# Kernel optimization log

Measured on AMD Instinct MI355X. Metric: run time of the kernel, lower is better.

Reference implementation:

```python
import jax, jax.numpy as jnp
import numpy as np

N = 100000      # num nodes
E = 3200000     # num edges (avg degree 32)
F = 512         # num_features
D = 256         # args.dim
C = 64          # num_classes
K = 10          # APPNP iterations
ALPHA = 0.1


def setup_inputs() -> dict:
    key = jax.random.key(0)
    ks = jax.random.split(key, 6)
    x = jax.random.normal(ks[0], (N, F), dtype=jnp.float32)
    edge_index = jax.random.randint(ks[1], (2, E), 0, N, dtype=jnp.int64)
    edge_weight_train = jax.random.normal(ks[2], (E,), dtype=jnp.float32)
    x_weight = jnp.ones((F,), dtype=jnp.float32)
    W1 = jax.random.normal(ks[3], (F, D), dtype=jnp.float32) * 0.02
    b1 = jnp.zeros((D,), dtype=jnp.float32)
    W2 = jax.random.normal(ks[4], (D, C), dtype=jnp.float32) * 0.02
    b2 = jnp.zeros((C,), dtype=jnp.float32)
    return {"x": x, "edge_index": edge_index, "edge_weight_train": edge_weight_train,
            "x_weight": x_weight, "W1": W1, "b1": b1, "W2": W2, "b2": b2}


def reference(x, edge_index, edge_weight_train, x_weight, W1, b1, W2, b2):
    row, col = edge_index[0], edge_index[1]
    # adj_sparse branch: mask edges with |w|==0, weight = sigmoid(w).
    # Filtering edges == zeroing their weight (degrees and messages scale by w).
    edge_mask = jnp.abs(edge_weight_train) > 0
    w = jnp.where(edge_mask, jax.nn.sigmoid(edge_weight_train), 0.0)
    # gcn_norm with self-loops (fill value 1.0)
    loop = jnp.arange(N, dtype=row.dtype)
    row2 = jnp.concatenate([row, loop])
    col2 = jnp.concatenate([col, loop])
    w2 = jnp.concatenate([w, jnp.ones((N,), dtype=w.dtype)])
    deg = jax.ops.segment_sum(w2, col2, num_segments=N)
    dinv = jnp.where(deg > 0, jax.lax.rsqrt(jnp.maximum(deg, 1e-12)), 0.0)
    norm = dinv[row2] * w2 * dinv[col2]  # [E+N]

    # feature_sparse branch
    x_mask = (jnp.abs(x_weight) > 0).astype(x.dtype)
    xw = jax.nn.sigmoid(x_weight) * x_mask
    xin = x * xw  # broadcast over nodes

    h = jax.nn.relu(xin @ W1 + b1)          # [N, D] (dropout is eval no-op)
    z0 = h @ W2 + b2                        # [N, C]

    z = z0
    for _ in range(K):
        msg = z[row2] * norm[:, None]       # gather + scale, [E+N, C]
        agg = jax.ops.segment_sum(msg, col2, num_segments=N)
        z = (1.0 - ALPHA) * agg + ALPHA * z0
    return jax.nn.log_softmax(z, axis=1)
```

## Files before the change

kernel.cpp:

```cpp
#include <hip/hip_runtime.h>
#include <hip/hip_bf16.h>
#include <cstdint>
#include <cstddef>

#define ALPHA 0.1f
#define K_ITERS 10
#define NPART 8

typedef __attribute__((ext_vector_type(8))) short bf16x8;
typedef __attribute__((ext_vector_type(4))) float f32x4;
typedef __attribute__((ext_vector_type(4))) unsigned int u32x4;

#define U15INV (1.0f / 32767.0f)

__device__ __forceinline__ unsigned short f2bf(float f) {
    unsigned int u = __float_as_uint(f);
    u += 0x7fffu + ((u >> 16) & 1u);
    return (unsigned short)(u >> 16);
}
__device__ __forceinline__ float bflo(unsigned int u) {
    return __uint_as_float(u << 16);
}
__device__ __forceinline__ float bfhi(unsigned int u) {
    return __uint_as_float(u & 0xffff0000u);
}
__device__ __forceinline__ unsigned int pack2(float a, float b) {
    return (unsigned int)f2bf(a) | ((unsigned int)f2bf(b) << 16);
}
__device__ __forceinline__ unsigned int u15q(float w) {
    return (unsigned int)(w * 32767.0f + 0.5f);
}
__device__ __forceinline__ int xcd_id() {
    unsigned int x;
    asm volatile("s_getreg_b32 %0, hwreg(20, 0, 32)" : "=s"(x));
    return (int)(x & (NPART - 1));
}


__global__ __launch_bounds__(256) void setup_k(int* cntp, unsigned int* cs, int* flag,
                                               int ncnt, int ncs) {
    int i = blockIdx.x * 256 + threadIdx.x;
    if (i == 0) *flag = 0;
    if (i < ncnt) cntp[i] = 0;
    if (i < ncs) cs[i] = 0;
}

__global__ void detect_idx_k(const void* ei, int* flag, int E_, int N_) {
    int tid = threadIdx.x;
    const long long* p = (const long long*)ei;
    int bad = 0;
    int lim = (E_ < 4096) ? E_ : 4096;
    for (int i = tid; i < lim; i += 256) {
        long long v = p[i];
        if (v < 0 || v >= (long long)N_) bad = 1;
    }
    if (bad) atomicOr(flag, 1);
}

__global__ __launch_bounds__(256) void wprep_k(const float* W1, const float* xw, unsigned short* W1bT,
                                               const float* W2, unsigned short* W2bT,
                                               int F_, int D_, int C_) {
    int i = blockIdx.x * 256 + threadIdx.x;
    int n1 = F_ * D_;
    if (i < n1) {
        int k = i / D_, n = i % D_;
        float t = xw[k];
        float s = (fabsf(t) > 0.0f) ? 1.0f / (1.0f + expf(-t)) : 0.0f;
        W1bT[(size_t)n * F_ + k] = f2bf(W1[i] * s);
    } else if (i < n1 + D_ * C_) {
        int j = i - n1;
        int k = j / C_, n = j % C_;
        W2bT[(size_t)n * D_ + k] = f2bf(W2[j]);
    }
}

__global__ __launch_bounds__(512) void mlp_prep_k(
        const float* __restrict__ A, const unsigned short* __restrict__ BT,
        const float* __restrict__ b1, const unsigned short* __restrict__ W2bT,
        const float* __restrict__ b2, unsigned short* __restrict__ z0out,
        int M, int K, int Nn, int Cn, int gx,
        const void* __restrict__ ei, const float* __restrict__ ew,
        unsigned long long* __restrict__ epack, int* __restrict__ cntp,
        const int* __restrict__ flag, int E_, int N_) {
    __shared__ __align__(16) unsigned short SMEM[32768];

    if (blockIdx.x >= gx) {
        int e = (blockIdx.x - gx) * 512 + threadIdx.x;
        if (e >= E_) return;
        int is32 = *flag;
        unsigned long long r, c;
        if (is32) {
            const int* p = (const int*)ei;
            r = (unsigned long long)(unsigned int)p[e];
            c = (unsigned long long)(unsigned int)p[(size_t)E_ + e];
        } else {
            const long long* p = (const long long*)ei;
            r = (unsigned long long)p[e];
            c = (unsigned long long)p[(size_t)E_ + e];
        }
        float t = ew[e];
        float wv = (fabsf(t) > 0.0f) ? 1.0f / (1.0f + expf(-t)) : 0.0f;
        unsigned long long part = (unsigned long long)xcd_id();
        unsigned long long rk = (unsigned long long)(unsigned int)
            __hip_atomic_fetch_add(&cntp[(size_t)part * N_ + (int)c], 1,
                                   __ATOMIC_RELAXED, __HIP_MEMORY_SCOPE_WORKGROUP);
        epack[e] = r | (c << 17) | ((unsigned long long)u15q(wv) << 34)
                     | (part << 49) | (rk << 52);
        return;
    }

    const int BK = 32;
    typedef unsigned short (*AslT)[4][128][8];
    typedef unsigned short (*BslT)[4][256][8];
    AslT Asl = (AslT)SMEM;
    BslT Bsl = (BslT)(SMEM + 8192);

    int tid = threadIdx.x;
    int row0 = blockIdx.x * 128;
    int wid = tid >> 6, lane = tid & 63;
    int wm = wid & 1, wn = wid >> 1;
    int lrow = lane & 15, kg = lane >> 4;

    f32x4 acc[4][4];
    #pragma unroll
    for (int i = 0; i < 4; ++i)
        #pragma unroll
        for (int j = 0; j < 4; ++j) acc[i][j] = (f32x4){0.f, 0.f, 0.f, 0.f};

    int ar = tid >> 2, akg = tid & 3;
    int agrow = row0 + ar;
    bool avalid = agrow < M;
    int bn_ = tid >> 1, bkh = (tid & 1) * 16;

    float fa[8];
    bf16x8 bv0, bv1;

    auto loadTile = [&](int k0) {
        if (avalid) {
            const f32x4* p = (const f32x4*)&A[(size_t)agrow * K + k0 + akg * 8];
            *(f32x4*)&fa[0] = p[0];
            *(f32x4*)&fa[4] = p[1];
        }
        const bf16x8* p = (const bf16x8*)&BT[(size_t)bn_ * K + k0 + bkh];
        bv0 = p[0]; bv1 = p[1];
    };
    auto stageTile = [&](int buf) {
        unsigned short av[8];
        #pragma unroll
        for (int q = 0; q < 8; ++q) av[q] = avalid ? f2bf(fa[q]) : (unsigned short)0;
        *(bf16x8*)&Asl[buf][akg][ar][0] = *(bf16x8*)&av[0];
        *(bf16x8*)&Bsl[buf][(bkh >> 3) + 0][bn_][0] = bv0;
        *(bf16x8*)&Bsl[buf][(bkh >> 3) + 1][bn_][0] = bv1;
    };

    int nsteps = K / BK;
    loadTile(0);
    stageTile(0);
    __syncthreads();

    int cur = 0;
    for (int step = 0; step < nsteps; ++step) {
        bool more = (step + 1) < nsteps;
        if (more) loadTile((step + 1) * BK);

        bf16x8 af[4], bfr[4];
        #pragma unroll
        for (int i = 0; i < 4; ++i)
            af[i] = *(bf16x8*)&Asl[cur][kg][wm * 64 + i * 16 + lrow][0];
        #pragma unroll
        for (int j = 0; j < 4; ++j)
            bfr[j] = *(bf16x8*)&Bsl[cur][kg][wn * 64 + j * 16 + lrow][0];
        #pragma unroll
        for (int i = 0; i < 4; ++i)
            #pragma unroll
            for (int j = 0; j < 4; ++j)
                acc[i][j] = __builtin_amdgcn_mfma_f32_16x16x32_bf16(af[i], bfr[j], acc[i][j], 0, 0, 0);

        if (more) stageTile(cur ^ 1);
        __syncthreads();
        cur ^= 1;
    }

    #pragma unroll
    for (int i = 0; i < 4; ++i) {
        #pragma unroll
        for (int j = 0; j < 4; ++j) {
            int k2 = wn * 64 + j * 16 + lrow;
            float bv = b1[k2];
            int base = ((k2 >> 5) * 4 + ((k2 >> 3) & 3)) * 1024 + (k2 & 7);
            #pragma unroll
            for (int r = 0; r < 4; ++r) {
                int row = wm * 64 + i * 16 + kg * 4 + r;
                float v = fmaxf(acc[i][j][r] + bv, 0.0f);
                SMEM[base + row * 8] = f2bf(v);
            }
        }
    }
    __syncthreads();

    f32x4 acc2[4];
    #pragma unroll
    for (int i = 0; i < 4; ++i) acc2[i] = (f32x4){0.f, 0.f, 0.f, 0.f};
    int col2 = wn * 16 + lrow;
    #pragma unroll
    for (int ch = 0; ch < 8; ++ch) {
        bf16x8 bfr2 = *(const bf16x8*)&W2bT[(size_t)col2 * Nn + ch * 32 + kg * 8];
        bf16x8 af2[4];
        #pragma unroll
        for (int i = 0; i < 4; ++i)
            af2[i] = *(bf16x8*)&SMEM[(ch * 4 + kg) * 1024 + (wm * 64 + i * 16 + lrow) * 8];
        #pragma unroll
        for (int i = 0; i < 4; ++i)
            acc2[i] = __builtin_amdgcn_mfma_f32_16x16x32_bf16(af2[i], bfr2, acc2[i], 0, 0, 0);
    }
    float bv2 = b2[col2];
    #pragma unroll
    for (int i = 0; i < 4; ++i) {
        #pragma unroll
        for (int r = 0; r < 4; ++r) {
            int grow = row0 + wm * 64 + i * 16 + kg * 4 + r;
            if (grow < M)
                z0out[(size_t)grow * Cn + col2] = f2bf(acc2[i][r] + bv2);
        }
    }
}

__global__ __launch_bounds__(256) void combine_k(const int* cntp, int* pofs, int* cnt8, int N_) {
    int i = blockIdx.x * 256 + threadIdx.x;
    if (i >= N_) return;
    int s = 0;
    #pragma unroll
    for (int p = 0; p < NPART; ++p) {
        size_t idx = (size_t)p * N_ + i;
        int v = cntp[idx];
        pofs[idx] = s;
        s += v;
    }
    cnt8[i] = (s + 7) & ~7;
}

__global__ __launch_bounds__(256) void scan1_k(const int* cnt, int* bsum, int N_) {
    __shared__ int sm[256];
    int t = threadIdx.x, i = blockIdx.x * 256 + t;
    sm[t] = (i < N_) ? cnt[i] : 0;
    __syncthreads();
    for (int off = 128; off; off >>= 1) {
        if (t < off) sm[t] += sm[t + off];
        __syncthreads();
    }
    if (t == 0) bsum[blockIdx.x] = sm[0];
}

__global__ __launch_bounds__(1024) void scan2_k(const int* bsum, int* boff, int nb) {
    __shared__ int sm[1024];
    int t = threadIdx.x;
    int v = (t < nb) ? bsum[t] : 0;
    sm[t] = v;
    __syncthreads();
    for (int off = 1; off < 1024; off <<= 1) {
        int x = (t >= off) ? sm[t - off] : 0;
        __syncthreads();
        sm[t] += x;
        __syncthreads();
    }
    if (t < nb) boff[t] = sm[t] - v;
}

__global__ __launch_bounds__(256) void scan3_k(const int* cnt, const int* boff, int* rowstart, int N_) {
    __shared__ int sm[256];
    int t = threadIdx.x, i = blockIdx.x * 256 + t;
    int v = (i < N_) ? cnt[i] : 0;
    sm[t] = v;
    __syncthreads();
    for (int off = 1; off < 256; off <<= 1) {
        int x = (t >= off) ? sm[t - off] : 0;
        __syncthreads();
        sm[t] += x;
        __syncthreads();
    }
    if (i < N_)  rowstart[i]  = boff[blockIdx.x] + sm[t] - v;
    if (i == N_ - 1) rowstart[N_] = boff[blockIdx.x] + sm[t];
}

__global__ __launch_bounds__(256) void fill_csr_k(const unsigned long long* epack, const int* pofs,
                                                  const int* rowstart, unsigned int* cs,
                                                  int E_, int N_) {
    int e = blockIdx.x * 256 + threadIdx.x;
    if (e >= E_) return;
    unsigned long long v = epack[e];
    unsigned int r   = (unsigned int)(v & 0x1ffffu);
    int          c   = (int)((v >> 17) & 0x1ffffu);
    unsigned int w15 = (unsigned int)((v >> 34) & 0x7fffu);
    int         part = (int)((v >> 49) & 7u);
    int           rk = (int)(v >> 52);
    int pos = rowstart[c] + pofs[(size_t)part * N_ + c] + rk;
    cs[pos] = r | (w15 << 17);
}

__global__ __launch_bounds__(256) void deg_dinv_k(const unsigned int* __restrict__ cs,
                                                  const int* __restrict__ rowstart,
                                                  float* __restrict__ dinv, int N_) {
    int node = blockIdx.x * 8 + (threadIdx.x >> 5);
    int l = threadIdx.x & 31;
    if (node >= N_) return;
    int s = rowstart[node], e = rowstart[node + 1];
    float sum = 0.0f;
    for (int j = s + l; j < e; j += 32) sum += (float)(cs[j] >> 17) * U15INV;
    #pragma unroll
    for (int off = 16; off; off >>= 1) sum += __shfl_xor(sum, off, 64);
    float d = sum + 1.0f;
    if (l == 0) dinv[node] = (d > 0.0f) ? rsqrtf(fmaxf(d, 1e-12f)) : 0.0f;
}

__global__ __launch_bounds__(256) void norm_k(unsigned int* __restrict__ cs,
                                              const int* __restrict__ rowstart,
                                              const float* __restrict__ dinv, int N_) {
    int node = blockIdx.x * 8 + (threadIdx.x >> 5);
    int l = threadIdx.x & 31;
    if (node >= N_) return;
    int s = rowstart[node], e = rowstart[node + 1];
    float dc = dinv[node];
    for (int j = s + l; j < e; j += 32) {
        unsigned int v = cs[j];
        unsigned int src = v & 0x1ffffu;
        float w = (float)(v >> 17) * U15INV;
        float nm = dinv[src] * w * dc;
        cs[j] = src | (u15q(nm) << 17);
    }
}

template<bool LAST>
__global__ __launch_bounds__(256) void prop8_k(const unsigned short* __restrict__ z,
                                               const unsigned short* __restrict__ z0,
                                               const int* __restrict__ rowstart,
                                               const unsigned int* __restrict__ cs,
                                               const float* __restrict__ dinv,
                                               unsigned short* __restrict__ znew,
                                               float* __restrict__ out, int N_) {
    int node = blockIdx.x * 32 + (threadIdx.x >> 3);
    int l = threadIdx.x & 7;
    if (node >= N_) return;
    int s = rowstart[node], e = rowstart[node + 1];
    float d = dinv[node];
    size_t ro = (size_t)node * 64 + l * 8;
    u32x4 zs = *(const u32x4*)&z[ro];
    float dd = d * d;
    float a[8];
    a[0] = dd * bflo(zs.x); a[1] = dd * bfhi(zs.x);
    a[2] = dd * bflo(zs.y); a[3] = dd * bfhi(zs.y);
    a[4] = dd * bflo(zs.z); a[5] = dd * bfhi(zs.z);
    a[6] = dd * bflo(zs.w); a[7] = dd * bfhi(zs.w);

    for (int j = s; j < e; j += 8) {
        u32x4 p0 = __builtin_nontemporal_load((const u32x4*)&cs[j]);
        u32x4 p1 = __builtin_nontemporal_load((const u32x4*)&cs[j + 4]);
        unsigned int pe[8] = { p0.x, p0.y, p0.z, p0.w, p1.x, p1.y, p1.z, p1.w };
        u32x4 g[8];
        #pragma unroll
        for (int q = 0; q < 8; ++q)
            g[q] = *(const u32x4*)&z[(size_t)(pe[q] & 0x1ffffu) * 64 + l * 8];
        #pragma unroll
        for (int q = 0; q < 8; ++q) {
            float w = (float)(pe[q] >> 17) * U15INV;
            a[0] += w * bflo(g[q].x); a[1] += w * bfhi(g[q].x);
            a[2] += w * bflo(g[q].y); a[3] += w * bfhi(g[q].y);
            a[4] += w * bflo(g[q].z); a[5] += w * bfhi(g[q].z);
            a[6] += w * bflo(g[q].w); a[7] += w * bfhi(g[q].w);
        }
    }

    u32x4 z0v = __builtin_nontemporal_load((const u32x4*)&z0[ro]);
    float v[8];
    float z0f[8] = { bflo(z0v.x), bfhi(z0v.x), bflo(z0v.y), bfhi(z0v.y),
                     bflo(z0v.z), bfhi(z0v.z), bflo(z0v.w), bfhi(z0v.w) };
    #pragma unroll
    for (int q = 0; q < 8; ++q) v[q] = (1.0f - ALPHA) * a[q] + ALPHA * z0f[q];

    if (!LAST) {
        u32x4 o;
        o.x = pack2(v[0], v[1]); o.y = pack2(v[2], v[3]);
        o.z = pack2(v[4], v[5]); o.w = pack2(v[6], v[7]);
        *(u32x4*)&znew[ro] = o;
    } else {
        float m = v[0];
        #pragma unroll
        for (int q = 1; q < 8; ++q) m = fmaxf(m, v[q]);
        #pragma unroll
        for (int off = 1; off < 8; off <<= 1) m = fmaxf(m, __shfl_xor(m, off, 64));
        float sum = 0.0f;
        #pragma unroll
        for (int q = 0; q < 8; ++q) sum += expf(v[q] - m);
        #pragma unroll
        for (int off = 1; off < 8; off <<= 1) sum += __shfl_xor(sum, off, 64);
        float lg = logf(sum);
        float4 o0 = make_float4(v[0] - m - lg, v[1] - m - lg, v[2] - m - lg, v[3] - m - lg);
        float4 o1 = make_float4(v[4] - m - lg, v[5] - m - lg, v[6] - m - lg, v[7] - m - lg);
        *(float4*)&out[ro] = o0;
        *(float4*)&out[ro + 4] = o1;
    }
}


extern "C" void kernel_launch(void* const* d_in, const int* in_sizes, int n_in,
                              void* d_out, int out_size, void* d_ws, size_t ws_size,
                              hipStream_t stream) {
    const float* x   = (const float*)d_in[0];
    const void*  ei  = d_in[1];
    const float* ew  = (const float*)d_in[2];
    const float* xw  = (const float*)d_in[3];
    const float* W1  = (const float*)d_in[4];
    const float* b1  = (const float*)d_in[5];
    const float* W2  = (const float*)d_in[6];
    const float* b2  = (const float*)d_in[7];

    const int F_ = in_sizes[3];
    const int N_ = in_sizes[0] / F_;
    const int E_ = in_sizes[2];
    const int D_ = in_sizes[5];
    const int C_ = in_sizes[7];

    const int E8 = E_ + 7 * N_;

    char* base = (char*)d_ws;
    size_t off = 0;
    auto take = [&](size_t bytes) -> void* {
        void* p = base + off;
        off += (bytes + 255) & ~(size_t)255;
        return p;
    };
    unsigned long long* epack = (unsigned long long*)take((size_t)E_ * 8);
    unsigned int* cs = (unsigned int*)take((size_t)E8 * 4);
    int*   cntp     = (int*)  take((size_t)NPART * N_ * 4);
    int*   pofs     = (int*)  take((size_t)NPART * N_ * 4);
    int*   cnt8     = (int*)  take((size_t)N_ * 4);
    float* dinv     = (float*)take((size_t)N_ * 4);
    int*   rowstart = (int*)  take((size_t)(N_ + 1) * 4);
    int*   flag     = (int*)  take(256);
    int*   bsum     = (int*)  take(4096 * 4);
    int*   boff     = (int*)  take(4096 * 4);
    unsigned short* W1bT = (unsigned short*)take((size_t)F_ * D_ * 2);
    unsigned short* W2bT = (unsigned short*)take((size_t)D_ * C_ * 2);
    unsigned short* z0b  = (unsigned short*)take((size_t)N_ * C_ * 2);
    unsigned short* za   = (unsigned short*)take((size_t)N_ * C_ * 2);
    unsigned short* zb   = (unsigned short*)take((size_t)N_ * C_ * 2);

    (void)ws_size; (void)n_in; (void)out_size;

    int nblk = (N_ + 255) / 256;
    int eblk = (E_ + 255) / 256;
    int ncnt = NPART * N_;
    int setup_blk = ((ncnt > E8 ? ncnt : E8) + 255) / 256;

    setup_k<<<setup_blk, 256, 0, stream>>>(cntp, cs, flag, ncnt, E8);
    detect_idx_k<<<1, 256, 0, stream>>>(ei, flag, E_, N_);
    wprep_k<<<(F_ * D_ + D_ * C_ + 255) / 256, 256, 0, stream>>>(W1, xw, W1bT, W2, W2bT, F_, D_, C_);

    int gx = (N_ + 127) / 128;
    int eblk512 = (E_ + 511) / 512;
    mlp_prep_k<<<gx + eblk512, 512, 0, stream>>>(
        x, W1bT, b1, W2bT, b2, z0b, N_, F_, D_, C_, gx,
        ei, ew, epack, cntp, flag, E_, N_);

    combine_k<<<nblk, 256, 0, stream>>>(cntp, pofs, cnt8, N_);
    scan1_k<<<nblk, 256, 0, stream>>>(cnt8, bsum, N_);
    scan2_k<<<1, 1024, 0, stream>>>(bsum, boff, nblk);
    scan3_k<<<nblk, 256, 0, stream>>>(cnt8, boff, rowstart, N_);
    fill_csr_k<<<eblk, 256, 0, stream>>>(epack, pofs, rowstart, cs, E_, N_);
    int gblk8 = (N_ + 7) / 8;
    deg_dinv_k<<<gblk8, 256, 0, stream>>>(cs, rowstart, dinv, N_);
    norm_k<<<gblk8, 256, 0, stream>>>(cs, rowstart, dinv, N_);

    int pblk = (N_ + 31) / 32;
    const unsigned short* cur = z0b;
    unsigned short* bufs[2] = { za, zb };
    for (int it = 0; it < K_ITERS - 1; ++it) {
        unsigned short* dst = bufs[it & 1];
        prop8_k<false><<<pblk, 256, 0, stream>>>(cur, z0b, rowstart, cs, dinv, dst, nullptr, N_);
        cur = dst;
    }
    prop8_k<true><<<pblk, 256, 0, stream>>>(cur, z0b, rowstart, cs, dinv, nullptr, (float*)d_out, N_);
}
```

Before: 839.0 us.

## Fuse norm into first propagation, merge scans, shrink MLP LDS, drop cs memset

Folds the separate edge-normalization pass into the first propagation iteration, which computes normalized weights on the fly, uses them, and writes them back to the CSR array for later iterations. Merges the block-sum scan into combine_k and zeroes only the CSR padding slots inside scan3_k instead of clearing the whole array in setup. Splits the second MLP GEMM into two halves over the hidden dimension so shared memory drops from 64KB to 48KB, which may allow more resident blocks. Saves kernel launches and full passes over cs, at the cost of extra syncs in the MLP epilogue and a heavier first propagation kernel.

```diff
diff --git a/kernel.cpp b/kernel.cpp
--- a/kernel.cpp
+++ b/kernel.cpp
@@ -37,12 +37,10 @@
 }
 
 
-__global__ __launch_bounds__(256) void setup_k(int* cntp, unsigned int* cs, int* flag,
-                                               int ncnt, int ncs) {
+__global__ __launch_bounds__(256) void setup_k(int* cntp, int* flag, int ncnt) {
     int i = blockIdx.x * 256 + threadIdx.x;
     if (i == 0) *flag = 0;
     if (i < ncnt) cntp[i] = 0;
-    if (i < ncs) cs[i] = 0;
 }
 
 __global__ void detect_idx_k(const void* ei, int* flag, int E_, int N_) {
@@ -82,7 +80,7 @@
         const void* __restrict__ ei, const float* __restrict__ ew,
         unsigned long long* __restrict__ epack, int* __restrict__ cntp,
         const int* __restrict__ flag, int E_, int N_) {
-    __shared__ __align__(16) unsigned short SMEM[32768];
+    __shared__ __align__(16) unsigned short SMEM[24576];
 
     if (blockIdx.x >= gx) {
         int e = (blockIdx.x - gx) * 512 + threadIdx.x;
@@ -181,38 +179,46 @@
         cur ^= 1;
     }
 
-    #pragma unroll
-    for (int i = 0; i < 4; ++i) {
-        #pragma unroll
-        for (int j = 0; j < 4; ++j) {
-            int k2 = wn * 64 + j * 16 + lrow;
-            float bv = b1[k2];
-            int base = ((k2 >> 5) * 4 + ((k2 >> 3) & 3)) * 1024 + (k2 & 7);
-            #pragma unroll
-            for (int r = 0; r < 4; ++r) {
-                int row = wm * 64 + i * 16 + kg * 4 + r;
-                float v = fmaxf(acc[i][j][r] + bv, 0.0f);
-                SMEM[base + row * 8] = f2bf(v);
-            }
-        }
-    }
-    __syncthreads();
-
     f32x4 acc2[4];
     #pragma unroll
     for (int i = 0; i < 4; ++i) acc2[i] = (f32x4){0.f, 0.f, 0.f, 0.f};
     int col2 = wn * 16 + lrow;
+
     #pragma unroll
-    for (int ch = 0; ch < 8; ++ch) {
-        bf16x8 bfr2 = *(const bf16x8*)&W2bT[(size_t)col2 * Nn + ch * 32 + kg * 8];
-        bf16x8 af2[4];
-        #pragma unroll
-        for (int i = 0; i < 4; ++i)
-            af2[i] = *(bf16x8*)&SMEM[(ch * 4 + kg) * 1024 + (wm * 64 + i * 16 + lrow) * 8];
-        #pragma unroll
-        for (int i = 0; i < 4; ++i)
-            acc2[i] = __builtin_amdgcn_mfma_f32_16x16x32_bf16(af2[i], bfr2, acc2[i], 0, 0, 0);
-    }
+    for (int p = 0; p < 2; ++p) {
+        if ((wn >> 1) == p) {
+            #pragma unroll
+            for (int i = 0; i < 4; ++i) {
+                #pragma unroll
+                for (int j = 0; j < 4; ++j) {
+                    int k2 = wn * 64 + j * 16 + lrow;
+                    int k2l = k2 - p * 128;
+                    float bv = b1[k2];
+                    int base = ((k2l >> 5) * 4 + ((k2l >> 3) & 3)) * 1024 + (k2l & 7);
+                    #pragma unroll
+                    for (int r = 0; r < 4; ++r) {
+                        int row = wm * 64 + i * 16 + kg * 4 + r;
+                        float v = fmaxf(acc[i][j][r] + bv, 0.0f);
+                        SMEM[base + row * 8] = f2bf(v);
+                    }
+                }
+            }
+        }
+        __syncthreads();
+        #pragma unroll
+        for (int ch = 0; ch < 4; ++ch) {
+            bf16x8 bfr2 = *(const bf16x8*)&W2bT[(size_t)col2 * Nn + p * 128 + ch * 32 + kg * 8];
+            bf16x8 af2[4];
+            #pragma unroll
+            for (int i = 0; i < 4; ++i)
+                af2[i] = *(bf16x8*)&SMEM[(ch * 4 + kg) * 1024 + (wm * 64 + i * 16 + lrow) * 8];
+            #pragma unroll
+            for (int i = 0; i < 4; ++i)
+                acc2[i] = __builtin_amdgcn_mfma_f32_16x16x32_bf16(af2[i], bfr2, acc2[i], 0, 0, 0);
+        }
+        __syncthreads();
+    }
+
     float bv2 = b2[col2];
     #pragma unroll
     for (int i = 0; i < 4; ++i) {
@@ -225,24 +231,26 @@
     }
 }
 
-__global__ __launch_bounds__(256) void combine_k(const int* cntp, int* pofs, int* cnt8, int N_) {
-    int i = blockIdx.x * 256 + threadIdx.x;
-    if (i >= N_) return;
-    int s = 0;
-    #pragma unroll
-    for (int p = 0; p < NPART; ++p) {
-        size_t idx = (size_t)p * N_ + i;
-        int v = cntp[idx];
-        pofs[idx] = s;
-        s += v;
-    }
-    cnt8[i] = (s + 7) & ~7;
-}
-
-__global__ __launch_bounds__(256) void scan1_k(const int* cnt, int* bsum, int N_) {
+__global__ __launch_bounds__(256) void combine_k(const int* cntp, int* pofs, int* cntT,
+                                                 int* cnt8, int* bsum, int N_) {
     __shared__ int sm[256];
-    int t = threadIdx.x, i = blockIdx.x * 256 + t;
-    sm[t] = (i < N_) ? cnt[i] : 0;
+    int t = threadIdx.x;
+    int i = blockIdx.x * 256 + t;
+    int c8 = 0;
+    if (i < N_) {
+        int s = 0;
+        #pragma unroll
+        for (int p = 0; p < NPART; ++p) {
+            size_t idx = (size_t)p * N_ + i;
+            int v = cntp[idx];
+            pofs[idx] = s;
+            s += v;
+        }
+        cntT[i] = s;
+        c8 = (s + 7) & ~7;
+        cnt8[i] = c8;
+    }
+    sm[t] = c8;
     __syncthreads();
     for (int off = 128; off; off >>= 1) {
         if (t < off) sm[t] += sm[t + off];
@@ -266,10 +274,11 @@
     if (t < nb) boff[t] = sm[t] - v;
 }
 
-__global__ __launch_bounds__(256) void scan3_k(const int* cnt, const int* boff, int* rowstart, int N_) {
+__global__ __launch_bounds__(256) void scan3_k(const int* cnt8, const int* cntT, const int* boff,
+                                               int* rowstart, unsigned int* cs, int N_) {
     __shared__ int sm[256];
     int t = threadIdx.x, i = blockIdx.x * 256 + t;
-    int v = (i < N_) ? cnt[i] : 0;
+    int v = (i < N_) ? cnt8[i] : 0;
     sm[t] = v;
     __syncthreads();
     for (int off = 1; off < 256; off <<= 1) {
@@ -278,7 +287,12 @@
         sm[t] += x;
         __syncthreads();
     }
-    if (i < N_)  rowstart[i]  = boff[blockIdx.x] + sm[t] - v;
+    if (i < N_) {
+        int base = boff[blockIdx.x] + sm[t] - v;
+        rowstart[i] = base;
+        int st = cntT[i];
+        for (int j = st; j < v; ++j) cs[base + j] = 0;
+    }
     if (i == N_ - 1) rowstart[N_] = boff[blockIdx.x] + sm[t];
 }
 
@@ -312,28 +326,11 @@
     if (l == 0) dinv[node] = (d > 0.0f) ? rsqrtf(fmaxf(d, 1e-12f)) : 0.0f;
 }
 
-__global__ __launch_bounds__(256) void norm_k(unsigned int* __restrict__ cs,
-                                              const int* __restrict__ rowstart,
-                                              const float* __restrict__ dinv, int N_) {
-    int node = blockIdx.x * 8 + (threadIdx.x >> 5);
-    int l = threadIdx.x & 31;
-    if (node >= N_) return;
-    int s = rowstart[node], e = rowstart[node + 1];
-    float dc = dinv[node];
-    for (int j = s + l; j < e; j += 32) {
-        unsigned int v = cs[j];
-        unsigned int src = v & 0x1ffffu;
-        float w = (float)(v >> 17) * U15INV;
-        float nm = dinv[src] * w * dc;
-        cs[j] = src | (u15q(nm) << 17);
-    }
-}
-
-template<bool LAST>
+template<int MODE>
 __global__ __launch_bounds__(256) void prop8_k(const unsigned short* __restrict__ z,
                                                const unsigned short* __restrict__ z0,
                                                const int* __restrict__ rowstart,
-                                               const unsigned int* __restrict__ cs,
+                                               unsigned int* __restrict__ cs,
                                                const float* __restrict__ dinv,
                                                unsigned short* __restrict__ znew,
                                                float* __restrict__ out, int N_) {
@@ -359,13 +356,37 @@
         #pragma unroll
         for (int q = 0; q < 8; ++q)
             g[q] = *(const u32x4*)&z[(size_t)(pe[q] & 0x1ffffu) * 64 + l * 8];
-        #pragma unroll
-        for (int q = 0; q < 8; ++q) {
-            float w = (float)(pe[q] >> 17) * U15INV;
-            a[0] += w * bflo(g[q].x); a[1] += w * bfhi(g[q].x);
-            a[2] += w * bflo(g[q].y); a[3] += w * bfhi(g[q].y);
-            a[4] += w * bflo(g[q].z); a[5] += w * bfhi(g[q].z);
-            a[6] += w * bflo(g[q].w); a[7] += w * bfhi(g[q].w);
+        if (MODE == 1) {
+            float dv[8];
+            #pragma unroll
+            for (int q = 0; q < 8; ++q) dv[q] = dinv[pe[q] & 0x1ffffu];
+            unsigned int ow[8];
+            #pragma unroll
+            for (int q = 0; q < 8; ++q) {
+                float wraw = (float)(pe[q] >> 17) * U15INV;
+                float nm = dv[q] * wraw * d;
+                ow[q] = (pe[q] & 0x1ffffu) | (u15q(nm) << 17);
+                a[0] += nm * bflo(g[q].x); a[1] += nm * bfhi(g[q].x);
+                a[2] += nm * bflo(g[q].y); a[3] += nm * bfhi(g[q].y);
+                a[4] += nm * bflo(g[q].z); a[5] += nm * bfhi(g[q].z);
+                a[6] += nm * bflo(g[q].w); a[7] += nm * bfhi(g[q].w);
+            }
+            if (l == 0) {
+                u32x4 o0, o1;
+                o0.x = ow[0]; o0.y = ow[1]; o0.z = ow[2]; o0.w = ow[3];
+                o1.x = ow[4]; o1.y = ow[5]; o1.z = ow[6]; o1.w = ow[7];
+                *(u32x4*)&cs[j] = o0;
+                *(u32x4*)&cs[j + 4] = o1;
+            }
+        } else {
+            #pragma unroll
+            for (int q = 0; q < 8; ++q) {
+                float w = (float)(pe[q] >> 17) * U15INV;
+                a[0] += w * bflo(g[q].x); a[1] += w * bfhi(g[q].x);
+                a[2] += w * bflo(g[q].y); a[3] += w * bfhi(g[q].y);
+                a[4] += w * bflo(g[q].z); a[5] += w * bfhi(g[q].z);
+                a[6] += w * bflo(g[q].w); a[7] += w * bfhi(g[q].w);
+            }
         }
     }
 
@@ -376,7 +397,7 @@
     #pragma unroll
     for (int q = 0; q < 8; ++q) v[q] = (1.0f - ALPHA) * a[q] + ALPHA * z0f[q];
 
-    if (!LAST) {
+    if (MODE != 2) {
         u32x4 o;
         o.x = pack2(v[0], v[1]); o.y = pack2(v[2], v[3]);
         o.z = pack2(v[4], v[5]); o.w = pack2(v[6], v[7]);
@@ -432,6 +453,7 @@
     unsigned int* cs = (unsigned int*)take((size_t)E8 * 4);
     int*   cntp     = (int*)  take((size_t)NPART * N_ * 4);
     int*   pofs     = (int*)  take((size_t)NPART * N_ * 4);
+    int*   cntT     = (int*)  take((size_t)N_ * 4);
     int*   cnt8     = (int*)  take((size_t)N_ * 4);
     float* dinv     = (float*)take((size_t)N_ * 4);
     int*   rowstart = (int*)  take((size_t)(N_ + 1) * 4);
@@ -449,9 +471,8 @@
     int nblk = (N_ + 255) / 256;
     int eblk = (E_ + 255) / 256;
     int ncnt = NPART * N_;
-    int setup_blk = ((ncnt > E8 ? ncnt : E8) + 255) / 256;
-
-    setup_k<<<setup_blk, 256, 0, stream>>>(cntp, cs, flag, ncnt, E8);
+
+    setup_k<<<(ncnt + 255) / 256, 256, 0, stream>>>(cntp, flag, ncnt);
     detect_idx_k<<<1, 256, 0, stream>>>(ei, flag, E_, N_);
     wprep_k<<<(F_ * D_ + D_ * C_ + 255) / 256, 256, 0, stream>>>(W1, xw, W1bT, W2, W2bT, F_, D_, C_);
 
@@ -461,22 +482,21 @@
         x, W1bT, b1, W2bT, b2, z0b, N_, F_, D_, C_, gx,
         ei, ew, epack, cntp, flag, E_, N_);
 
-    combine_k<<<nblk, 256, 0, stream>>>(cntp, pofs, cnt8, N_);
-    scan1_k<<<nblk, 256, 0, stream>>>(cnt8, bsum, N_);
+    combine_k<<<nblk, 256, 0, stream>>>(cntp, pofs, cntT, cnt8, bsum, N_);
     scan2_k<<<1, 1024, 0, stream>>>(bsum, boff, nblk);
-    scan3_k<<<nblk, 256, 0, stream>>>(cnt8, boff, rowstart, N_);
+    scan3_k<<<nblk, 256, 0, stream>>>(cnt8, cntT, boff, rowstart, cs, N_);
     fill_csr_k<<<eblk, 256, 0, stream>>>(epack, pofs, rowstart, cs, E_, N_);
     int gblk8 = (N_ + 7) / 8;
     deg_dinv_k<<<gblk8, 256, 0, stream>>>(cs, rowstart, dinv, N_);
-    norm_k<<<gblk8, 256, 0, stream>>>(cs, rowstart, dinv, N_);
 
     int pblk = (N_ + 31) / 32;
-    const unsigned short* cur = z0b;
     unsigned short* bufs[2] = { za, zb };
-    for (int it = 0; it < K_ITERS - 1; ++it) {
+    prop8_k<1><<<pblk, 256, 0, stream>>>(z0b, z0b, rowstart, cs, dinv, za, nullptr, N_);
+    const unsigned short* cur = za;
+    for (int it = 1; it < K_ITERS - 1; ++it) {
         unsigned short* dst = bufs[it & 1];
-        prop8_k<false><<<pblk, 256, 0, stream>>>(cur, z0b, rowstart, cs, dinv, dst, nullptr, N_);
+        prop8_k<0><<<pblk, 256, 0, stream>>>(cur, z0b, rowstart, cs, dinv, dst, nullptr, N_);
         cur = dst;
     }
-    prop8_k<true><<<pblk, 256, 0, stream>>>(cur, z0b, rowstart, cs, dinv, nullptr, (float*)d_out, N_);
-}
+    prop8_k<2><<<pblk, 256, 0, stream>>>(cur, z0b, rowstart, cs, dinv, nullptr, (float*)d_out, N_);
+}
```

Measured after the change: 843.9 us. Within noise of the previous version (+0.6%).
